# Kernel tuning notes

Measured on AMD Instinct MI355X. Metric: run time of the kernel, lower is better.

## Reference

```python
import jax, jax.numpy as jnp
import numpy as np
import math

B, S, HID = 2, 2048, 2048
H, HKV, D, L = 16, 4, 128, 64
THETA = 10000.0
N_REP = H // HKV


def _rope(t, pos, theta=THETA):
    # t: [B, h, S, D], pos: [B, S] int
    d = t.shape[-1]
    inv_freq = 1.0 / (theta ** (jnp.arange(0, d, 2, dtype=jnp.float32) / d))  # [d/2]
    ang = pos.astype(jnp.float32)[:, :, None] * inv_freq  # [B, S, d/2]
    cos = jnp.concatenate([jnp.cos(ang), jnp.cos(ang)], axis=-1)[:, None]  # [B,1,S,d]
    sin = jnp.concatenate([jnp.sin(ang), jnp.sin(ang)], axis=-1)[:, None]
    t1, t2 = t[..., : d // 2], t[..., d // 2 :]
    rot = jnp.concatenate([-t2, t1], axis=-1)
    return t * cos + rot * sin


def setup_inputs() -> dict:
    key = jax.random.key(0)
    ks = jax.random.split(key, 9)
    sc = lambda fin: 1.0 / math.sqrt(fin)
    x = jax.random.normal(ks[0], (B, S, HID), dtype=jnp.float32)
    position_ids = jnp.broadcast_to(jnp.arange(S, dtype=jnp.int32), (B, S))
    # additive causal mask [1,1,S,S]
    causal = jnp.triu(jnp.full((S, S), -1e9, dtype=jnp.float32), k=1)
    attention_mask = causal[None, None]
    Wq = jax.random.normal(ks[1], (HID, H * D), dtype=jnp.float32) * sc(HID)
    Wk = jax.random.normal(ks[2], (HID, HKV * D), dtype=jnp.float32) * sc(HID)
    Wv = jax.random.normal(ks[3], (HID, HKV * D), dtype=jnp.float32) * sc(HID)
    Wql = jax.random.normal(ks[4], (D, L), dtype=jnp.float32) * sc(D)
    Wkl = jax.random.normal(ks[5], (D, L), dtype=jnp.float32) * sc(D)
    Wvl = jax.random.normal(ks[6], (D, L), dtype=jnp.float32) * sc(D)
    Wo = jax.random.normal(ks[7], (H * D, HID), dtype=jnp.float32) * sc(H * D)
    return {"x": x, "position_ids": position_ids, "attention_mask": attention_mask,
            "Wq": Wq, "Wk": Wk, "Wv": Wv, "Wql": Wql, "Wkl": Wkl, "Wvl": Wvl, "Wo": Wo}


def reference(x, position_ids, attention_mask, Wq, Wk, Wv, Wql, Wkl, Wvl, Wo):
    b, s, _ = x.shape
    q = (x @ Wq).reshape(b, s, H, D).transpose(0, 2, 1, 3)    # [B,H,S,D]
    k = (x @ Wk).reshape(b, s, HKV, D).transpose(0, 2, 1, 3)  # [B,HKV,S,D]
    v = (x @ Wv).reshape(b, s, HKV, D).transpose(0, 2, 1, 3)
    q = _rope(q, position_ids)
    k = _rope(k, position_ids)
    # latent compression per head-dim
    q_l = jnp.einsum('bhsd,dl->bhsl', q, Wql)  # [B,H,S,L]
    k_l = jnp.einsum('bhsd,dl->bhsl', k, Wkl)  # [B,HKV,S,L]
    v_l = jnp.einsum('bhsd,dl->bhsl', v, Wvl)
    k_l = jnp.repeat(k_l, N_REP, axis=1)  # repeat_kv -> [B,H,S,L]
    v_l = jnp.repeat(v_l, N_REP, axis=1)
    scale = math.sqrt(L)
    attn = jnp.einsum('bhql,bhkl->bhqk', q_l, k_l) / scale
    attn = attn + attention_mask
    attn = jax.nn.softmax(attn, axis=-1)
    out = jnp.einsum('bhqk,bhkl->bhql', attn, v_l)  # [B,H,S,L]
    if L < D:
        out = jnp.pad(out, ((0, 0), (0, 0), (0, 0), (0, D - L)))
    out = out.transpose(0, 2, 1, 3).reshape(b, s, H * D)
    return out @ Wo
```

## Files before the change

kernel.cpp:

```cpp
#include <hip/hip_runtime.h>
#include <cstddef>

constexpr int kB   = 2;
constexpr int kS   = 2048;
constexpr int kHID = 2048;
constexpr int kH   = 16;
constexpr int kHKV = 4;
constexpr int kD   = 128;
constexpr int kL   = 64;
constexpr int kTok = kB * kS;
constexpr int kNQKV = kH * kD + 2 * kHKV * kD;

typedef __attribute__((ext_vector_type(8))) short bf16x8;
typedef __attribute__((ext_vector_type(4))) float f32x4;

static __device__ __forceinline__ short f2bf(float f) {
  union { float f; unsigned u; } v{f};
  const unsigned r = (v.u + 0x7fff + ((v.u >> 16) & 1)) >> 16;
  return (short)r;
}
static __device__ __forceinline__ float bf2f(short s) {
  union { unsigned u; float f; } v;
  v.u = ((unsigned)(unsigned short)s) << 16;
  return v.f;
}

static __device__ __forceinline__ bf16x8 pack8(float4 a, float4 b) {
  bf16x8 r;
  r[0] = f2bf(a.x); r[1] = f2bf(a.y); r[2] = f2bf(a.z); r[3] = f2bf(a.w);
  r[4] = f2bf(b.x); r[5] = f2bf(b.y); r[6] = f2bf(b.z); r[7] = f2bf(b.w);
  return r;
}

static __device__ __forceinline__ unsigned cvt_pk_bf16(float lo, float hi) {
  unsigned r;
  asm("v_cvt_pk_bf16_f32 %0, %1, %2" : "=v"(r) : "v"(lo), "v"(hi));
  return r;
}

typedef __attribute__((address_space(3))) void       lds_void;
typedef __attribute__((address_space(1))) const void gm_void;
static __device__ __forceinline__ void gload16(const void* g, void* l) {
  __builtin_amdgcn_global_load_lds((gm_void*)g, (lds_void*)l, 16, 0, 0);
}

static __device__ __forceinline__ int2 xcd_swz(int nx, int ny) {
  int wg = blockIdx.y * nx + blockIdx.x;
  const int cpx = (nx * ny) >> 3;
  wg = (wg & 7) * cpx + (wg >> 3);
  int2 r; r.x = wg % nx; r.y = wg / nx;
  return r;
}

__global__ __launch_bounds__(256) void cvt_bf16(const float* __restrict__ in,
                                                short* __restrict__ out, int n8) {
  const int i = blockIdx.x * 256 + threadIdx.x;
  if (i >= n8) return;
  const float4 a = *(const float4*)&in[i * 8];
  const float4 b = *(const float4*)&in[i * 8 + 4];
  *(bf16x8*)&out[i * 8] = pack8(a, b);
}

__global__ __launch_bounds__(256) void trig_table(const int* __restrict__ pos,
                                                  float* __restrict__ tbl) {
  const int idx = blockIdx.x * 256 + threadIdx.x;
  if (idx >= kTok * 64) return;
  const int i = idx & 63, t = idx >> 6;
  const float p = (float)pos[t];
  const float inv_freq = expf(-(float)i * (9.210340371976184f / 64.0f));
  const float ang = p * inv_freq;
  tbl[t * 128 + i]      = cosf(ang);
  tbl[t * 128 + 64 + i] = sinf(ang);
}

__global__ __launch_bounds__(256) void transpose_qkv(
    const float* __restrict__ Wq, const float* __restrict__ Wk,
    const float* __restrict__ Wv, short* __restrict__ out) {
  __shared__ float T[64][65];
  const int n0 = blockIdx.x * 64, k0 = blockIdx.y * 64;
  const float* in; int Nin, nl0;
  if (n0 < 2048)      { in = Wq; Nin = 2048; nl0 = n0; }
  else if (n0 < 2560) { in = Wk; Nin = 512;  nl0 = n0 - 2048; }
  else                { in = Wv; Nin = 512;  nl0 = n0 - 2560; }
  const int tid = threadIdx.x;
  const int rr = tid >> 4, cc = tid & 15;
#pragma unroll
  for (int ii = 0; ii < 4; ++ii) {
    const int kr = rr + ii * 16;
    const float4 v = *(const float4*)&in[(size_t)(k0 + kr) * Nin + nl0 + cc * 4];
    T[kr][cc * 4 + 0] = v.x; T[kr][cc * 4 + 1] = v.y;
    T[kr][cc * 4 + 2] = v.z; T[kr][cc * 4 + 3] = v.w;
  }
  __syncthreads();
#pragma unroll
  for (int ii = 0; ii < 4; ++ii) {
    const int n = rr + ii * 16;
    const short4 s4 = make_short4(f2bf(T[cc * 4 + 0][n]), f2bf(T[cc * 4 + 1][n]),
                                  f2bf(T[cc * 4 + 2][n]), f2bf(T[cc * 4 + 3][n]));
    *(short4*)&out[(size_t)(n0 + n) * kHID + k0 + cc * 4] = s4;
  }
}

template <bool REMAP>
__global__ __launch_bounds__(256) void transpose_cvt(
    const float* __restrict__ in, short* __restrict__ out,
    int Nin, int out_ld, int row_off, float scale) {
  __shared__ float T[64][65];
  const int tid = threadIdx.x;
  const int k0 = blockIdx.y * 64, n0 = blockIdx.x * 64;
  const int rr = tid >> 4;
  const int cc = tid & 15;
#pragma unroll
  for (int ii = 0; ii < 4; ++ii) {
    const int kr = rr + ii * 16;
    int gr = k0 + kr;
    if (REMAP) gr = ((gr >> 6) << 7) + (gr & 63);
    const float4 v = *(const float4*)&in[(size_t)gr * Nin + n0 + cc * 4];
    T[kr][cc * 4 + 0] = v.x * scale; T[kr][cc * 4 + 1] = v.y * scale;
    T[kr][cc * 4 + 2] = v.z * scale; T[kr][cc * 4 + 3] = v.w * scale;
  }
  __syncthreads();
#pragma unroll
  for (int ii = 0; ii < 4; ++ii) {
    const int n = rr + ii * 16;
    const short4 s4 = make_short4(f2bf(T[cc * 4 + 0][n]), f2bf(T[cc * 4 + 1][n]),
                                  f2bf(T[cc * 4 + 2][n]), f2bf(T[cc * 4 + 3][n]));
    *(short4*)&out[(size_t)(row_off + n0 + n) * out_ld + k0 + cc * 4] = s4;
  }
}

__global__ __launch_bounds__(256) void transpose_lat3(
    const float* __restrict__ Wql, const float* __restrict__ Wkl,
    const float* __restrict__ Wvl, short* __restrict__ WqlT,
    short* __restrict__ WklT, short* __restrict__ WvlT) {
  __shared__ float T[64][65];
  const float* in; short* out; float scale;
  if (blockIdx.z == 0)      { in = Wql; out = WqlT; scale = 0.125f; }
  else if (blockIdx.z == 1) { in = Wkl; out = WklT; scale = 1.0f; }
  else                      { in = Wvl; out = WvlT; scale = 1.0f; }
  const int tid = threadIdx.x;
  const int k0 = blockIdx.y * 64;
  const int rr = tid >> 4, cc = tid & 15;
#pragma unroll
  for (int ii = 0; ii < 4; ++ii) {
    const int kr = rr + ii * 16;
    const float4 v = *(const float4*)&in[(size_t)(k0 + kr) * kL + cc * 4];
    T[kr][cc * 4 + 0] = v.x * scale; T[kr][cc * 4 + 1] = v.y * scale;
    T[kr][cc * 4 + 2] = v.z * scale; T[kr][cc * 4 + 3] = v.w * scale;
  }
  __syncthreads();
#pragma unroll
  for (int ii = 0; ii < 4; ++ii) {
    const int n = rr + ii * 16;
    const short4 s4 = make_short4(f2bf(T[cc * 4 + 0][n]), f2bf(T[cc * 4 + 1][n]),
                                  f2bf(T[cc * 4 + 2][n]), f2bf(T[cc * 4 + 3][n]));
    *(short4*)&out[(size_t)n * kD + k0 + cc * 4] = s4;
  }
}

__global__ __launch_bounds__(512) void gemm_qkv8(
    const short* __restrict__ A, const short* __restrict__ Bt,
    short* __restrict__ C0, short* __restrict__ C1, short* __restrict__ C2,
    int K) {
  __shared__ short As[2][256 * 64];
  __shared__ short Bs[2][256 * 64];
  const int tid = threadIdx.x;
  const int lane = tid & 63, w = tid >> 6;
  const int lr = lane & 15, lk = lane >> 4;
  const int wm = w >> 2, wn = w & 3;
  const int2 sw = xcd_swz(kNQKV / 256, kTok / 256);
  const int row0 = sw.y * 256, col0 = sw.x * 256;
  const int NT = K >> 6;

  auto stage = [&](int kt) {
    const int b = kt & 1;
    const int k0 = kt << 6;
#pragma unroll
    for (int j = 0; j < 4; ++j) {
      const int idx = j * 512 + tid;
      const int row = idx >> 3, blk = idx & 7;
      const int gcol = k0 + ((blk ^ (row & 7)) << 3);
      gload16(A + (size_t)(row0 + row) * K + gcol, &As[b][row * 64 + blk * 8]);
    }
#pragma unroll
    for (int j = 0; j < 4; ++j) {
      const int idx = j * 512 + tid;
      const int row = idx >> 3, blk = idx & 7;
      const int gcol = k0 + ((blk ^ (row & 7)) << 3);
      gload16(Bt + (size_t)(col0 + row) * K + gcol, &Bs[b][row * 64 + blk * 8]);
    }
  };

  f32x4 acc[8][4] = {};

  stage(0);
  for (int t = 0; t < NT; ++t) {
    const int b = t & 1;
    if (t + 1 < NT) {
      stage(t + 1);
      asm volatile("s_waitcnt vmcnt(8)" ::: "memory");
    } else {
      asm volatile("s_waitcnt vmcnt(0)" ::: "memory");
    }
    __builtin_amdgcn_s_barrier();

    bf16x8 bb[4][2];
#pragma unroll
    for (int n = 0; n < 4; ++n) {
      const int row = wn * 64 + n * 16 + lr;
#pragma unroll
      for (int ch = 0; ch < 2; ++ch) {
        const int blk = (ch * 4 + lk) ^ (row & 7);
        bb[n][ch] = *(const bf16x8*)&Bs[b][row * 64 + blk * 8];
      }
    }
#pragma unroll
    for (int qm = 0; qm < 2; ++qm) {
      bf16x8 a[4][2];
#pragma unroll
      for (int j = 0; j < 4; ++j) {
        const int row = wm * 128 + (qm * 4 + j) * 16 + lr;
#pragma unroll
        for (int ch = 0; ch < 2; ++ch) {
          const int blk = (ch * 4 + lk) ^ (row & 7);
          a[j][ch] = *(const bf16x8*)&As[b][row * 64 + blk * 8];
        }
      }
      __builtin_amdgcn_s_setprio(1);
#pragma unroll
      for (int j = 0; j < 4; ++j)
#pragma unroll
        for (int n = 0; n < 4; ++n)
#pragma unroll
          for (int ch = 0; ch < 2; ++ch)
            acc[qm * 4 + j][n] = __builtin_amdgcn_mfma_f32_16x16x32_bf16(
                a[j][ch], bb[n][ch], acc[qm * 4 + j][n], 0, 0, 0);
      __builtin_amdgcn_s_setprio(0);
    }
    __builtin_amdgcn_s_barrier();
  }

  short* dst; int ld, cb;
  if (col0 < 2048)      { dst = C0; ld = 2048; cb = col0; }
  else if (col0 < 2560) { dst = C1; ld = 512;  cb = col0 - 2048; }
  else                  { dst = C2; ld = 512;  cb = col0 - 2560; }
  const int crow0 = row0 + wm * 128 + lk * 4;
  const int ccol0 = cb + wn * 64 + lr;
#pragma unroll
  for (int mf = 0; mf < 8; ++mf)
#pragma unroll
    for (int nf = 0; nf < 4; ++nf)
#pragma unroll
      for (int r = 0; r < 4; ++r)
        dst[(size_t)(crow0 + mf * 16 + r) * ld + ccol0 + nf * 16] =
            f2bf(acc[mf][nf][r]);
}

__global__ __launch_bounds__(512) void gemm_out8(
    const short* __restrict__ A, const short* __restrict__ Bt,
    float* __restrict__ C, int M, int N, int K) {
  __shared__ short As[2][256 * 64];
  __shared__ short Bs[2][128 * 64];
  const int tid = threadIdx.x;
  const int lane = tid & 63, w = tid >> 6;
  const int lr = lane & 15, lk = lane >> 4;
  const int wm = w >> 2, wn = w & 3;
  const int2 sw = xcd_swz(N / 128, M / 256);
  const int row0 = sw.y * 256, col0 = sw.x * 128;
  const int NT = K >> 6;

  auto stage = [&](int kt) {
    const int b = kt & 1;
    const int k0 = kt << 6;
#pragma unroll
    for (int j = 0; j < 4; ++j) {
      const int idx = j * 512 + tid;
      const int row = idx >> 3, blk = idx & 7;
      const int gcol = k0 + ((blk ^ (row & 7)) << 3);
      gload16(A + (size_t)(row0 + row) * K + gcol, &As[b][row * 64 + blk * 8]);
    }
#pragma unroll
    for (int j = 0; j < 2; ++j) {
      const int idx = j * 512 + tid;
      const int row = idx >> 3, blk = idx & 7;
      const int gcol = k0 + ((blk ^ (row & 7)) << 3);
      gload16(Bt + (size_t)(col0 + row) * K + gcol, &Bs[b][row * 64 + blk * 8]);
    }
  };

  f32x4 acc[8][2] = {};

  stage(0);
  for (int t = 0; t < NT; ++t) {
    const int b = t & 1;
    if (t + 1 < NT) {
      stage(t + 1);
      asm volatile("s_waitcnt vmcnt(6)" ::: "memory");
    } else {
      asm volatile("s_waitcnt vmcnt(0)" ::: "memory");
    }
    __builtin_amdgcn_s_barrier();

    bf16x8 bb[2][2];
#pragma unroll
    for (int n = 0; n < 2; ++n) {
      const int row = wn * 32 + n * 16 + lr;
#pragma unroll
      for (int ch = 0; ch < 2; ++ch) {
        const int blk = (ch * 4 + lk) ^ (row & 7);
        bb[n][ch] = *(const bf16x8*)&Bs[b][row * 64 + blk * 8];
      }
    }
#pragma unroll
    for (int qm = 0; qm < 2; ++qm) {
      bf16x8 a[4][2];
#pragma unroll
      for (int j = 0; j < 4; ++j) {
        const int row = wm * 128 + (qm * 4 + j) * 16 + lr;
#pragma unroll
        for (int ch = 0; ch < 2; ++ch) {
          const int blk = (ch * 4 + lk) ^ (row & 7);
          a[j][ch] = *(const bf16x8*)&As[b][row * 64 + blk * 8];
        }
      }
      __builtin_amdgcn_s_setprio(1);
#pragma unroll
      for (int j = 0; j < 4; ++j)
#pragma unroll
        for (int n = 0; n < 2; ++n)
#pragma unroll
          for (int ch = 0; ch < 2; ++ch)
            acc[qm * 4 + j][n] = __builtin_amdgcn_mfma_f32_16x16x32_bf16(
                a[j][ch], bb[n][ch], acc[qm * 4 + j][n], 0, 0, 0);
      __builtin_amdgcn_s_setprio(0);
    }
    __builtin_amdgcn_s_barrier();
  }

  const int crow0 = row0 + wm * 128 + lk * 4;
  const int ccol0 = col0 + wn * 32 + lr;
#pragma unroll
  for (int mf = 0; mf < 8; ++mf)
#pragma unroll
    for (int nf = 0; nf < 2; ++nf)
#pragma unroll
      for (int r = 0; r < 4; ++r)
        C[(size_t)(crow0 + mf * 16 + r) * N + ccol0 + nf * 16] = acc[mf][nf][r];
}

__global__ __launch_bounds__(256) void rope_latent_all(
    const short* __restrict__ qb, const short* __restrict__ kb,
    const short* __restrict__ vb, const short* __restrict__ WqlT,
    const short* __restrict__ WklT, const short* __restrict__ WvlT,
    const float* __restrict__ tbl, short* __restrict__ q_l,
    short* __restrict__ k_l, short* __restrict__ v_lT) {
  __shared__ short Tw[4][1280];
  const int yz = blockIdx.y;
  const short* in; const short* WT; short* out; int nh; bool ROPE, TR;
  int bh;
  if (yz < 32)      { in = qb; WT = WqlT; out = q_l;  nh = kH;   ROPE = true;  TR = false; bh = yz; }
  else if (yz < 40) { in = kb; WT = WklT; out = k_l;  nh = kHKV; ROPE = true;  TR = false; bh = yz - 32; }
  else              { in = vb; WT = WvlT; out = v_lT; nh = kHKV; ROPE = false; TR = true;  bh = yz - 40; }

  const int tid = threadIdx.x;
  const int lane = tid & 63;
  const int w = tid >> 6;
  const int lr = lane & 15;
  const int lk = lane >> 4;
  const int b = bh / nh, h = bh % nh;
  const int s0 = blockIdx.x * 64;
  const int srow = s0 + w * 16 + lr;
  const int tok = b * kS + srow;

  const short* ip = in + ((size_t)tok * nh + h) * kD + lk * 8;
  bf16x8 raw[4];
#pragma unroll
  for (int ch = 0; ch < 4; ++ch) raw[ch] = *(const bf16x8*)(ip + ch * 32);

  bf16x8 af[4];
  if (ROPE) {
    float a[4][8];
#pragma unroll
    for (int ch = 0; ch < 4; ++ch)
#pragma unroll
      for (int i = 0; i < 8; ++i) a[ch][i] = bf2f(raw[ch][i]);
    const float* tb = tbl + (size_t)tok * 128;
    float c[2][8], sn[2][8];
#pragma unroll
    for (int g = 0; g < 2; ++g) {
      const float4 cA = *(const float4*)(tb + g * 32 + lk * 8);
      const float4 cB = *(const float4*)(tb + g * 32 + lk * 8 + 4);
      const float4 sA = *(const float4*)(tb + 64 + g * 32 + lk * 8);
      const float4 sB = *(const float4*)(tb + 64 + g * 32 + lk * 8 + 4);
      c[g][0] = cA.x; c[g][1] = cA.y; c[g][2] = cA.z; c[g][3] = cA.w;
      c[g][4] = cB.x; c[g][5] = cB.y; c[g][6] = cB.z; c[g][7] = cB.w;
      sn[g][0] = sA.x; sn[g][1] = sA.y; sn[g][2] = sA.z; sn[g][3] = sA.w;
      sn[g][4] = sB.x; sn[g][5] = sB.y; sn[g][6] = sB.z; sn[g][7] = sB.w;
    }
    float o[4][8];
#pragma unroll
    for (int g = 0; g < 2; ++g)
#pragma unroll
      for (int i = 0; i < 8; ++i) {
        o[g][i]     = a[g][i]     * c[g][i] - a[g + 2][i] * sn[g][i];
        o[g + 2][i] = a[g + 2][i] * c[g][i] + a[g][i]     * sn[g][i];
      }
#pragma unroll
    for (int ch = 0; ch < 4; ++ch)
#pragma unroll
      for (int i = 0; i < 8; ++i) af[ch][i] = f2bf(o[ch][i]);
  } else {
#pragma unroll
    for (int ch = 0; ch < 4; ++ch) af[ch] = raw[ch];
  }

  f32x4 acc[4] = {};
#pragma unroll
  for (int cb = 0; cb < 4; ++cb) {
#pragma unroll
    for (int ch = 0; ch < 4; ++ch) {
      const bf16x8 bfrag =
          *(const bf16x8*)&WT[(size_t)(cb * 16 + lr) * kD + ch * 32 + lk * 8];
      acc[cb] = __builtin_amdgcn_mfma_f32_16x16x32_bf16(af[ch], bfrag,
                                                        acc[cb], 0, 0, 0);
    }
  }

  short* T = Tw[w];
  if (!TR) {
#pragma unroll
    for (int cb = 0; cb < 4; ++cb)
#pragma unroll
      for (int r = 0; r < 4; ++r)
        T[(lk * 4 + r) * 72 + cb * 16 + lr] = f2bf(acc[cb][r]);
    asm volatile("s_waitcnt lgkmcnt(0)" ::: "memory");
#pragma unroll
    for (int it = 0; it < 2; ++it) {
      const int idx = it * 64 + lane;
      const int row = idx >> 3, c8 = (idx & 7) << 3;
      *(bf16x8*)&out[((size_t)bh * kS + s0 + w * 16 + row) * kL + c8] =
          *(const bf16x8*)&T[row * 72 + c8];
    }
  } else {
#pragma unroll
    for (int cb = 0; cb < 4; ++cb)
#pragma unroll
      for (int r = 0; r < 4; ++r)
        T[(cb * 16 + lr) * 20 + lk * 4 + r] = f2bf(acc[cb][r]);
    asm volatile("s_waitcnt lgkmcnt(0)" ::: "memory");
    const size_t orow = ((size_t)bh * kL + lane) * kS + s0 + w * 16;
#pragma unroll
    for (int c = 0; c < 4; ++c)
      *(short4*)&out[orow + c * 4] = *(const short4*)&T[lane * 20 + c * 4];
  }
}

__global__ __launch_bounds__(512) void flash_attn_mfma(
    const short* __restrict__ ql, const short* __restrict__ kl,
    const short* __restrict__ vlT, short* __restrict__ attn_out) {
  constexpr int LDK = 72;
  __shared__ short Kt[2][64 * LDK];
  __shared__ short Vt[2][64 * LDK];
  __shared__ short Pt[128 * LDK];

  const int tid = threadIdx.x;
  const int lane = tid & 63;
  const int w = tid >> 6;
  const int lr = lane & 15;
  const int lk = lane >> 4;
  const int bid = blockIdx.y;
  const int bx = (bid < 8) ? (2 * bid) : (31 - 2 * bid);
  const int q0 = bx * 128;
  const int bh = blockIdx.x;
  const int b = bh >> 4, h = bh & 15;
  const int hk = h >> 2;
  const int wrow = q0 + w * 16;

  const short* qrow = ql + ((size_t)bh * kS + wrow + lr) * kL;
  bf16x8 qf[2];
  qf[0] = *(const bf16x8*)(qrow + lk * 8);
  qf[1] = *(const bf16x8*)(qrow + 32 + lk * 8);

  f32x4 Of[4] = {};
  float m_r[4], l_r[4];
#pragma unroll
  for (int r = 0; r < 4; ++r) { m_r[r] = -3.0e38f; l_r[r] = 0.f; }

  const size_t kbase = (size_t)(b * kHKV + hk) * kS * kL;
  const size_t vbase = (size_t)(b * kHKV + hk) * kL * kS;
  const int ntiles = q0 / 64 + 2;
  const int sr = tid >> 3, sc8 = (tid & 7) << 3;
  const short* kp = kl + kbase + (size_t)sr * kL + sc8;
  const short* vp = vlT + vbase + (size_t)sr * kS + sc8;

  *(bf16x8*)&Kt[0][sr * LDK + sc8] = *(const bf16x8*)kp;
  *(bf16x8*)&Vt[0][sr * LDK + sc8] = *(const bf16x8*)vp;
  __syncthreads();

  int cur = 0;
  for (int t = 0; t < ntiles; ++t) {
    const int j0 = t * 64;
    const bool pre = (t + 1 < ntiles);
    bf16x8 krn, vrn;
    if (pre) {
      krn = *(const bf16x8*)(kp + (size_t)(j0 + 64) * kL);
      vrn = *(const bf16x8*)(vp + (j0 + 64));
    }

    if (j0 <= wrow) {
      const short* Kc = &Kt[cur][0];
      const short* Vc = &Vt[cur][0];

      f32x4 Sf[4];
      __builtin_amdgcn_s_setprio(1);
#pragma unroll
      for (int cb = 0; cb < 4; ++cb) {
        f32x4 acc = {};
#pragma unroll
        for (int ch = 0; ch < 2; ++ch) {
          const bf16x8 kf = *(const bf16x8*)&Kc[(cb * 16 + lr) * LDK + ch * 32 + lk * 8];
          acc = __builtin_amdgcn_mfma_f32_16x16x32_bf16(qf[ch], kf, acc, 0, 0, 0);
        }
        Sf[cb] = acc;
      }
      __builtin_amdgcn_s_setprio(0);

      float mt[4] = {-3.0e38f, -3.0e38f, -3.0e38f, -3.0e38f};
      if (j0 + 63 > wrow) {
#pragma unroll
        for (int cb = 0; cb < 4; ++cb)
#pragma unroll
          for (int r = 0; r < 4; ++r) {
            float s = Sf[cb][r];
            if ((j0 + cb * 16 + lr) > (wrow + lk * 4 + r)) s = -3.0e38f;
            Sf[cb][r] = s;
            mt[r] = fmaxf(mt[r], s);
          }
      } else {
#pragma unroll
        for (int cb = 0; cb < 4; ++cb)
#pragma unroll
          for (int r = 0; r < 4; ++r) mt[r] = fmaxf(mt[r], Sf[cb][r]);
      }
#pragma unroll
      for (int d = 1; d < 16; d <<= 1)
#pragma unroll
        for (int r = 0; r < 4; ++r) mt[r] = fmaxf(mt[r], __shfl_xor(mt[r], d));

      const bool need = (mt[0] > m_r[0] + 8.f) || (mt[1] > m_r[1] + 8.f) ||
                        (mt[2] > m_r[2] + 8.f) || (mt[3] > m_r[3] + 8.f);
      const bool resc = __any((int)need);
      float corr[4] = {1.f, 1.f, 1.f, 1.f};
      if (resc) {
#pragma unroll
        for (int r = 0; r < 4; ++r) {
          const float mnew = fmaxf(m_r[r], mt[r]);
          corr[r] = __expf(m_r[r] - mnew);
          m_r[r] = mnew;
          l_r[r] *= corr[r];
        }
      }
#pragma unroll
      for (int cb = 0; cb < 4; ++cb) {
        const float p0 = __expf(Sf[cb][0] - m_r[0]);
        const float p1 = __expf(Sf[cb][1] - m_r[1]);
        const float p2 = __expf(Sf[cb][2] - m_r[2]);
        const float p3 = __expf(Sf[cb][3] - m_r[3]);
        l_r[0] += p0; l_r[1] += p1; l_r[2] += p2; l_r[3] += p3;
        const unsigned pk01 = cvt_pk_bf16(p0, p1);
        const unsigned pk23 = cvt_pk_bf16(p2, p3);
        short* prow = &Pt[(w * 16 + lk * 4) * LDK + cb * 16 + lr];
        prow[0 * LDK] = (short)(pk01 & 0xffff);
        prow[1 * LDK] = (short)(pk01 >> 16);
        prow[2 * LDK] = (short)(pk23 & 0xffff);
        prow[3 * LDK] = (short)(pk23 >> 16);
      }
      asm volatile("s_waitcnt lgkmcnt(0)" ::: "memory");

      __builtin_amdgcn_s_setprio(1);
#pragma unroll
      for (int cb = 0; cb < 4; ++cb) {
        f32x4 acc = Of[cb];
        if (resc) {
#pragma unroll
          for (int r = 0; r < 4; ++r) acc[r] *= corr[r];
        }
#pragma unroll
        for (int ch = 0; ch < 2; ++ch) {
          const bf16x8 pf = *(const bf16x8*)&Pt[(w * 16 + lr) * LDK + ch * 32 + lk * 8];
          const bf16x8 vf = *(const bf16x8*)&Vc[(cb * 16 + lr) * LDK + ch * 32 + lk * 8];
          acc = __builtin_amdgcn_mfma_f32_16x16x32_bf16(pf, vf, acc, 0, 0, 0);
        }
        Of[cb] = acc;
      }
      __builtin_amdgcn_s_setprio(0);
    }

    if (pre) {
      *(bf16x8*)&Kt[cur ^ 1][sr * LDK + sc8] = krn;
      *(bf16x8*)&Vt[cur ^ 1][sr * LDK + sc8] = vrn;
    }
    __syncthreads();
    cur ^= 1;
  }

#pragma unroll
  for (int d = 1; d < 16; d <<= 1)
#pragma unroll
    for (int r = 0; r < 4; ++r) l_r[r] += __shfl_xor(l_r[r], d);

#pragma unroll
  for (int r = 0; r < 4; ++r) {
    const float inv = 1.f / l_r[r];
    const size_t row = (size_t)(b * kS + wrow + lk * 4 + r) * (kH * kL);
#pragma unroll
    for (int cb = 0; cb < 4; ++cb)
      attn_out[row + h * kL + cb * 16 + lr] = f2bf(Of[cb][r] * inv);
  }
}

extern "C" void kernel_launch(void* const* d_in, const int* in_sizes, int n_in,
                              void* d_out, int out_size, void* d_ws, size_t ws_size,
                              hipStream_t stream) {
  const float* x    = (const float*)d_in[0];
  const int*   pos  = (const int*)d_in[1];
  const float* Wq   = (const float*)d_in[3];
  const float* Wk   = (const float*)d_in[4];
  const float* Wv   = (const float*)d_in[5];
  const float* Wql  = (const float*)d_in[6];
  const float* Wkl  = (const float*)d_in[7];
  const float* Wvl  = (const float*)d_in[8];
  const float* Wo   = (const float*)d_in[9];
  float* out = (float*)d_out;

  char* p = (char*)d_ws;
  short* x_bf  = (short*)p; p += (size_t)kTok * kHID * 2;
  short* Wqkv  = (short*)p; p += (size_t)kNQKV * kHID * 2;
  short* WoT   = (short*)p; p += (size_t)kHID * (kH * kL) * 2;
  short* WqlT  = (short*)p; p += (size_t)kL * kD * 2;
  short* WklT  = (short*)p; p += (size_t)kL * kD * 2;
  short* WvlT  = (short*)p; p += (size_t)kL * kD * 2;
  float* tbl   = (float*)p; p += (size_t)kTok * 128 * 4;
  short* k_buf = (short*)p; p += (size_t)kTok * kHKV * kD * 2;
  short* v_buf = (short*)p; p += (size_t)kTok * kHKV * kD * 2;
  short* q_l   = (short*)p; p += (size_t)kB * kH * kS * kL * 2;
  short* k_l   = (short*)p; p += (size_t)kB * kHKV * kS * kL * 2;
  short* v_lT  = (short*)p; p += (size_t)kB * kHKV * kS * kL * 2;
  short* attn  = (short*)p;
  short* q_buf = (short*)d_out;

  cvt_bf16<<<kTok * kHID / 8 / 256, 256, 0, stream>>>(x, x_bf, kTok * kHID / 8);
  trig_table<<<kTok * 64 / 256, 256, 0, stream>>>(pos, tbl);
  transpose_qkv<<<dim3(kNQKV / 64, kHID / 64), 256, 0, stream>>>(
      Wq, Wk, Wv, Wqkv);
  transpose_cvt<true><<<dim3(kHID / 64, (kH * kL) / 64), 256, 0, stream>>>(
      Wo, WoT, kHID, kH * kL, 0, 1.0f);
  transpose_lat3<<<dim3(1, kD / 64, 3), 256, 0, stream>>>(
      Wql, Wkl, Wvl, WqlT, WklT, WvlT);

  gemm_qkv8<<<dim3(kNQKV / 256, kTok / 256), 512, 0, stream>>>(
      x_bf, Wqkv, q_buf, k_buf, v_buf, kHID);

  rope_latent_all<<<dim3(kS / 64, 48), 256, 0, stream>>>(
      q_buf, k_buf, v_buf, WqlT, WklT, WvlT, tbl, q_l, k_l, v_lT);

  flash_attn_mfma<<<dim3(kB * kH, kS / 128), 512, 0, stream>>>(
      q_l, k_l, v_lT, attn);

  gemm_out8<<<dim3(kHID / 128, kTok / 256), 512, 0, stream>>>(
      attn, WoT, out, kTok, kHID, kH * kL);
}
```

Baseline: 200.1 us.

## Transpose attention MFMA operands to keep P in registers via lane shuffles

Swaps the MFMA operand order so S^T and O^T are computed, which gives each lane one query row. The row max and sum then need only two cross-lane shuffles, and a single scalar running max and sum per lane replaces the four per-row values. The P tile is redistributed to the PV MFMA layout with __shfl instead of a round trip through the Pt shared buffer and its lgkmcnt wait, which also lowers LDS use. The output store becomes short4 vector writes, at the cost of extra shuffle and select instructions.

```diff
diff --git a/kernel.cpp b/kernel.cpp
--- a/kernel.cpp
+++ b/kernel.cpp
@@ -461,7 +461,6 @@
   constexpr int LDK = 72;
   __shared__ short Kt[2][64 * LDK];
   __shared__ short Vt[2][64 * LDK];
-  __shared__ short Pt[128 * LDK];
 
   const int tid = threadIdx.x;
   const int lane = tid & 63;
@@ -482,9 +481,7 @@
   qf[1] = *(const bf16x8*)(qrow + 32 + lk * 8);
 
   f32x4 Of[4] = {};
-  float m_r[4], l_r[4];
-#pragma unroll
-  for (int r = 0; r < 4; ++r) { m_r[r] = -3.0e38f; l_r[r] = 0.f; }
+  float m = -3.0e38f, l = 0.f;
 
   const size_t kbase = (size_t)(b * kHKV + hk) * kS * kL;
   const size_t vbase = (size_t)(b * kHKV + hk) * kL * kS;
@@ -496,6 +493,9 @@
   *(bf16x8*)&Kt[0][sr * LDK + sc8] = *(const bf16x8*)kp;
   *(bf16x8*)&Vt[0][sr * LDK + sc8] = *(const bf16x8*)vp;
   __syncthreads();
+
+  const int sl0 = lr + ((lane & 16) << 1);
+  const bool hi = (lk >> 1) != 0;
 
   int cur = 0;
   for (int t = 0; t < ntiles; ++t) {
@@ -519,81 +519,79 @@
 #pragma unroll
         for (int ch = 0; ch < 2; ++ch) {
           const bf16x8 kf = *(const bf16x8*)&Kc[(cb * 16 + lr) * LDK + ch * 32 + lk * 8];
-          acc = __builtin_amdgcn_mfma_f32_16x16x32_bf16(qf[ch], kf, acc, 0, 0, 0);
+          acc = __builtin_amdgcn_mfma_f32_16x16x32_bf16(kf, qf[ch], acc, 0, 0, 0);
         }
         Sf[cb] = acc;
       }
       __builtin_amdgcn_s_setprio(0);
 
-      float mt[4] = {-3.0e38f, -3.0e38f, -3.0e38f, -3.0e38f};
+      float mt = -3.0e38f;
       if (j0 + 63 > wrow) {
 #pragma unroll
         for (int cb = 0; cb < 4; ++cb)
 #pragma unroll
           for (int r = 0; r < 4; ++r) {
             float s = Sf[cb][r];
-            if ((j0 + cb * 16 + lr) > (wrow + lk * 4 + r)) s = -3.0e38f;
+            if ((j0 + cb * 16 + lk * 4 + r) > (wrow + lr)) s = -3.0e38f;
             Sf[cb][r] = s;
-            mt[r] = fmaxf(mt[r], s);
+            mt = fmaxf(mt, s);
           }
       } else {
 #pragma unroll
         for (int cb = 0; cb < 4; ++cb)
 #pragma unroll
-          for (int r = 0; r < 4; ++r) mt[r] = fmaxf(mt[r], Sf[cb][r]);
-      }
-#pragma unroll
-      for (int d = 1; d < 16; d <<= 1)
-#pragma unroll
-        for (int r = 0; r < 4; ++r) mt[r] = fmaxf(mt[r], __shfl_xor(mt[r], d));
-
-      const bool need = (mt[0] > m_r[0] + 8.f) || (mt[1] > m_r[1] + 8.f) ||
-                        (mt[2] > m_r[2] + 8.f) || (mt[3] > m_r[3] + 8.f);
-      const bool resc = __any((int)need);
-      float corr[4] = {1.f, 1.f, 1.f, 1.f};
+          for (int r = 0; r < 4; ++r) mt = fmaxf(mt, Sf[cb][r]);
+      }
+      mt = fmaxf(mt, __shfl_xor(mt, 16));
+      mt = fmaxf(mt, __shfl_xor(mt, 32));
+
+      const bool resc = __any((int)(mt > m + 8.f));
       if (resc) {
-#pragma unroll
-        for (int r = 0; r < 4; ++r) {
-          const float mnew = fmaxf(m_r[r], mt[r]);
-          corr[r] = __expf(m_r[r] - mnew);
-          m_r[r] = mnew;
-          l_r[r] *= corr[r];
+        const float mnew = fmaxf(m, mt);
+        const float corr = __expf(m - mnew);
+        m = mnew;
+        l *= corr;
+#pragma unroll
+        for (int lb = 0; lb < 4; ++lb)
+#pragma unroll
+          for (int r = 0; r < 4; ++r) Of[lb][r] *= corr;
+      }
+
+      unsigned pk[4][2];
+#pragma unroll
+      for (int cb = 0; cb < 4; ++cb) {
+        const float p0 = __expf(Sf[cb][0] - m);
+        const float p1 = __expf(Sf[cb][1] - m);
+        const float p2 = __expf(Sf[cb][2] - m);
+        const float p3 = __expf(Sf[cb][3] - m);
+        l += (p0 + p1) + (p2 + p3);
+        pk[cb][0] = cvt_pk_bf16(p0, p1);
+        pk[cb][1] = cvt_pk_bf16(p2, p3);
+      }
+
+#pragma unroll
+      for (int ch = 0; ch < 2; ++ch) {
+        const unsigned lo00 = __shfl(pk[2 * ch][0], sl0);
+        const unsigned lo01 = __shfl(pk[2 * ch][1], sl0);
+        const unsigned lo10 = __shfl(pk[2 * ch][0], sl0 + 16);
+        const unsigned lo11 = __shfl(pk[2 * ch][1], sl0 + 16);
+        const unsigned hi00 = __shfl(pk[2 * ch + 1][0], sl0);
+        const unsigned hi01 = __shfl(pk[2 * ch + 1][1], sl0);
+        const unsigned hi10 = __shfl(pk[2 * ch + 1][0], sl0 + 16);
+        const unsigned hi11 = __shfl(pk[2 * ch + 1][1], sl0 + 16);
+        union { unsigned u[4]; bf16x8 v; } pf;
+        pf.u[0] = hi ? hi00 : lo00;
+        pf.u[1] = hi ? hi01 : lo01;
+        pf.u[2] = hi ? hi10 : lo10;
+        pf.u[3] = hi ? hi11 : lo11;
+        __builtin_amdgcn_s_setprio(1);
+#pragma unroll
+        for (int lb = 0; lb < 4; ++lb) {
+          const bf16x8 vf = *(const bf16x8*)&Vc[(lb * 16 + lr) * LDK + ch * 32 + lk * 8];
+          Of[lb] = __builtin_amdgcn_mfma_f32_16x16x32_bf16(vf, pf.v, Of[lb], 0, 0, 0);
         }
-      }
-#pragma unroll
-      for (int cb = 0; cb < 4; ++cb) {
-        const float p0 = __expf(Sf[cb][0] - m_r[0]);
-        const float p1 = __expf(Sf[cb][1] - m_r[1]);
-        const float p2 = __expf(Sf[cb][2] - m_r[2]);
-        const float p3 = __expf(Sf[cb][3] - m_r[3]);
-        l_r[0] += p0; l_r[1] += p1; l_r[2] += p2; l_r[3] += p3;
-        const unsigned pk01 = cvt_pk_bf16(p0, p1);
-        const unsigned pk23 = cvt_pk_bf16(p2, p3);
-        short* prow = &Pt[(w * 16 + lk * 4) * LDK + cb * 16 + lr];
-        prow[0 * LDK] = (short)(pk01 & 0xffff);
-        prow[1 * LDK] = (short)(pk01 >> 16);
-        prow[2 * LDK] = (short)(pk23 & 0xffff);
-        prow[3 * LDK] = (short)(pk23 >> 16);
-      }
-      asm volatile("s_waitcnt lgkmcnt(0)" ::: "memory");
-
-      __builtin_amdgcn_s_setprio(1);
-#pragma unroll
-      for (int cb = 0; cb < 4; ++cb) {
-        f32x4 acc = Of[cb];
-        if (resc) {
-#pragma unroll
-          for (int r = 0; r < 4; ++r) acc[r] *= corr[r];
-        }
-#pragma unroll
-        for (int ch = 0; ch < 2; ++ch) {
-          const bf16x8 pf = *(const bf16x8*)&Pt[(w * 16 + lr) * LDK + ch * 32 + lk * 8];
-          const bf16x8 vf = *(const bf16x8*)&Vc[(cb * 16 + lr) * LDK + ch * 32 + lk * 8];
-          acc = __builtin_amdgcn_mfma_f32_16x16x32_bf16(pf, vf, acc, 0, 0, 0);
-        }
-        Of[cb] = acc;
-      }
-      __builtin_amdgcn_s_setprio(0);
+        __builtin_amdgcn_s_setprio(0);
+      }
     }
 
     if (pre) {
@@ -604,18 +602,16 @@
     cur ^= 1;
   }
 
-#pragma unroll
-  for (int d = 1; d < 16; d <<= 1)
-#pragma unroll
-    for (int r = 0; r < 4; ++r) l_r[r] += __shfl_xor(l_r[r], d);
-
-#pragma unroll
-  for (int r = 0; r < 4; ++r) {
-    const float inv = 1.f / l_r[r];
-    const size_t row = (size_t)(b * kS + wrow + lk * 4 + r) * (kH * kL);
-#pragma unroll
-    for (int cb = 0; cb < 4; ++cb)
-      attn_out[row + h * kL + cb * 16 + lr] = f2bf(Of[cb][r] * inv);
+  l += __shfl_xor(l, 16);
+  l += __shfl_xor(l, 32);
+  const float inv = 1.f / l;
+  const size_t rowoff =
+      (size_t)(b * kS + wrow + lr) * (kH * kL) + h * kL + lk * 4;
+#pragma unroll
+  for (int lb = 0; lb < 4; ++lb) {
+    const short4 s4 = make_short4(f2bf(Of[lb][0] * inv), f2bf(Of[lb][1] * inv),
+                                  f2bf(Of[lb][2] * inv), f2bf(Of[lb][3] * inv));
+    *(short4*)&attn_out[rowoff + lb * 16] = s4;
   }
 }
 
```

Result: faster. 194.1 us (-3.0%).
